# Kernel tuning notes

Measured on AMD Instinct MI355X. Metric: run time of the kernel, lower is better.

Reference implementation:

```python
import jax, jax.numpy as jnp
import numpy as np

B, T, D, M, N = 32, 24, 32, 32, 32
H = 32           # hidden_dim (must equal D due to .view in the torch code)
C = M * N        # number of independent per-cell LSTMs
K = 3            # conv kernel size, padding = K // 2


def setup_inputs() -> dict:
    key = jax.random.key(0)
    ks = jax.random.split(key, 7)
    s = 1.0 / np.sqrt(H)  # torch nn.LSTM default init scale
    return {
        "x": jax.random.normal(ks[0], (B, T, D, M, N), jnp.float32),
        "W_ih": jax.random.uniform(ks[1], (C, 4 * H, D), jnp.float32, -s, s),
        "W_hh": jax.random.uniform(ks[2], (C, 4 * H, H), jnp.float32, -s, s),
        "b_ih": jax.random.uniform(ks[3], (C, 4 * H), jnp.float32, -s, s),
        "b_hh": jax.random.uniform(ks[4], (C, 4 * H), jnp.float32, -s, s),
        "conv_w": jax.random.normal(ks[5], (1, H, K, K), jnp.float32) * 0.05,
        "conv_b": jax.random.normal(ks[6], (1,), jnp.float32) * 0.05,
    }


def _spatial_lstm(x, W_ih, W_hh, b_ih, b_hh):
    # x: (B,T,D,M,N) -> per-cell sequences (T,C,B,D)
    xf = x.reshape(B, T, D, C).transpose(1, 3, 0, 2)
    bias = (b_ih + b_hh)[:, None, :]  # (C,1,4H)

    def step(carry, xt):
        h, c = carry  # (C,B,H)
        g = (jnp.einsum('cbd,cgd->cbg', xt, W_ih)
             + jnp.einsum('cbh,cgh->cbg', h, W_hh) + bias)
        i, f, gg, o = jnp.split(g, 4, axis=-1)  # torch gate order i,f,g,o
        c = jax.nn.sigmoid(f) * c + jax.nn.sigmoid(i) * jnp.tanh(gg)
        h = jax.nn.sigmoid(o) * jnp.tanh(c)
        return (h, c), h

    h0 = jnp.zeros((C, B, H), x.dtype)
    _, hs = jax.lax.scan(step, (h0, h0), xf)  # hs: (T,C,B,H)
    # stack over cells, view back to grid: (B,T,H,M,N)
    return hs.transpose(2, 0, 3, 1).reshape(B, T, H, M, N)


def reference(x, W_ih, W_hh, b_ih, b_hh, conv_w, conv_b):
    spatial = _spatial_lstm(x, W_ih, W_hh, b_ih, b_hh)  # (B,T,H,M,N)
    y = jax.lax.conv_general_dilated(
        spatial.reshape(B * T, H, M, N), conv_w,
        window_strides=(1, 1), padding=[(K // 2, K // 2)] * 2,
        dimension_numbers=('NCHW', 'OIHW', 'NCHW'))
    y = y + conv_b[None, :, None, None]
    return jax.nn.sigmoid(y).reshape(B, T, -1, M, N)


if __name__ == "__main__":
    out = reference(**setup_inputs())
    print(out.shape)
```

## Files before the change

kernel.cpp:

```cpp
#include <hip/hip_runtime.h>

#define Bn 32
#define Tn 24
#define Dn 32
#define Hn 32
#define Cn 1024
#define DC (Dn*Cn)
#define TDC (Tn*Dn*Cn)
#define MP 34
#define PPXN (MP*MP)
#define IMGS (MP*MP*32)
#define SCALE 1.442695041f

typedef __attribute__((ext_vector_type(8))) short bf16x8;
typedef __attribute__((ext_vector_type(4))) float f32x4;

__device__ __forceinline__ unsigned cvt_pk(float lo, float hi) {
    unsigned r; asm("v_cvt_pk_bf16_f32 %0, %1, %2" : "=v"(r) : "v"(lo), "v"(hi)); return r;
}
__device__ __forceinline__ float lo16f(unsigned u) { return __builtin_bit_cast(float, u << 16); }
__device__ __forceinline__ float hi16f(unsigned u) { return __builtin_bit_cast(float, u & 0xffff0000u); }
__device__ __forceinline__ float rcp_(float x) { return __builtin_amdgcn_rcpf(x); }
__device__ __forceinline__ float exp2_(float x) { return __builtin_amdgcn_exp2f(x); }
__device__ __forceinline__ bf16x8 bc(int4 v) { return __builtin_bit_cast(bf16x8, v); }

struct __align__(16) LdsT {
    unsigned short Xh[2][2][32][48];
    unsigned short Xl[2][2][32][48];
    float Hf[2][2][32][36];
};

__global__ __launch_bounds__(512)
void zero_halo(unsigned short* __restrict__ sp) {
    int gid = blockIdx.x * 512 + threadIdx.x;
    if (gid >= 3072 * 132) return;
    int plane = gid / 132;
    int r = gid - plane * 132;
    int m, n;
    if (r < 34)       { m = 0;      n = r; }
    else if (r < 68)  { m = 33;     n = r - 34; }
    else if (r < 100) { m = r - 67; n = 0; }
    else              { m = r - 99; n = 33; }
    int4 z = {0, 0, 0, 0};
    *(int4*)(sp + ((size_t)plane * PPXN + m * MP + n) * 8) = z;
}

__global__ __launch_bounds__(256) __attribute__((amdgpu_waves_per_eu(3, 3)))
void lstm_k10(const float* __restrict__ x,
              const float* __restrict__ Wih,
              const float* __restrict__ Whh,
              const float* __restrict__ bih,
              const float* __restrict__ bhh,
              unsigned short* __restrict__ sp)
{
    __shared__ LdsT lds;
    const int tid  = threadIdx.x;
    const int lane = tid & 63;
    const int wave = tid >> 6;
    const int ci   = wave >> 1;
    const int half = wave & 1;
    const int l16  = lane & 15;
    const int kg   = lane >> 4;
    const int bid  = blockIdx.x;
    const int cellbase = (bid & 7) * 128 + (bid >> 3) * 2;
    const int cell = cellbase + ci;

    int4 wihh[4], wihl[4], whhh[4], whhl[4];
    float biasr[4];
#pragma unroll
    for (int q = 0; q < 4; ++q) {
        const int g = q * 32 + half * 16 + l16;
        const float* wp = Wih + (size_t)cell * 4096 + g * 32 + kg * 8;
        const float* hp = Whh + (size_t)cell * 4096 + g * 32 + kg * 8;
        float wv[8], hv[8];
#pragma unroll
        for (int j = 0; j < 8; ++j) { wv[j] = wp[j] * SCALE; hv[j] = hp[j] * SCALE; }
        unsigned a0 = cvt_pk(wv[0], wv[1]), a1 = cvt_pk(wv[2], wv[3]);
        unsigned a2 = cvt_pk(wv[4], wv[5]), a3 = cvt_pk(wv[6], wv[7]);
        wihh[q] = int4{(int)a0, (int)a1, (int)a2, (int)a3};
        wihl[q] = int4{(int)cvt_pk(wv[0] - lo16f(a0), wv[1] - hi16f(a0)),
                       (int)cvt_pk(wv[2] - lo16f(a1), wv[3] - hi16f(a1)),
                       (int)cvt_pk(wv[4] - lo16f(a2), wv[5] - hi16f(a2)),
                       (int)cvt_pk(wv[6] - lo16f(a3), wv[7] - hi16f(a3))};
        unsigned b0 = cvt_pk(hv[0], hv[1]), b1 = cvt_pk(hv[2], hv[3]);
        unsigned b2 = cvt_pk(hv[4], hv[5]), b3 = cvt_pk(hv[6], hv[7]);
        whhh[q] = int4{(int)b0, (int)b1, (int)b2, (int)b3};
        whhl[q] = int4{(int)cvt_pk(hv[0] - lo16f(b0), hv[1] - hi16f(b0)),
                       (int)cvt_pk(hv[2] - lo16f(b1), hv[3] - hi16f(b1)),
                       (int)cvt_pk(hv[4] - lo16f(b2), hv[5] - hi16f(b2)),
                       (int)cvt_pk(hv[6] - lo16f(b3), hv[7] - hi16f(b3))};
        biasr[q] = (bih[cell * 128 + g] + bhh[cell * 128 + g]) * SCALE;
    }

    const int sb = tid >> 3;
    const int d0 = (tid & 7) * 4;
    const float* xg0 = x + (size_t)sb * TDC + (size_t)d0 * Cn + cellbase;

    const int sm = cell >> 5, sn = cell & 31;
    const int ppx = (sm + 1) * MP + (sn + 1);
    unsigned short* spb = sp + ((size_t)(half * 16 + l16) * Tn * 4 + kg) * (PPXN * 8)
                             + (size_t)ppx * 8;

    float hD[8] = {};
    float cst[8] = {};
    float2 nx[4];
#pragma unroll
    for (int k = 0; k < 4; ++k) nx[k] = *(const float2*)(xg0 + k * Cn);

    for (int t = 0; t < Tn; ++t) {
        const int bufi = t & 1;
#pragma unroll
        for (int cc = 0; cc < 2; ++cc) {
            float f0 = cc ? nx[0].y : nx[0].x;
            float f1 = cc ? nx[1].y : nx[1].x;
            float f2 = cc ? nx[2].y : nx[2].x;
            float f3 = cc ? nx[3].y : nx[3].x;
            unsigned a0 = cvt_pk(f0, f1), a1 = cvt_pk(f2, f3);
            float r0 = f0 - lo16f(a0), r1 = f1 - hi16f(a0);
            float r2 = f2 - lo16f(a1), r3 = f3 - hi16f(a1);
            int2 hi2 = {(int)a0, (int)a1};
            int2 lo2 = {(int)cvt_pk(r0, r1), (int)cvt_pk(r2, r3)};
            *(int2*)&lds.Xh[bufi][cc][sb][d0] = hi2;
            *(int2*)&lds.Xl[bufi][cc][sb][d0] = lo2;
        }
#pragma unroll
        for (int i = 0; i < 8; ++i) {
            int mt = i >> 2, r = i & 3;
            lds.Hf[bufi][ci][mt * 16 + kg * 4 + r][half * 16 + l16] = hD[i];
        }
        if (t < Tn - 1) {
#pragma unroll
            for (int k = 0; k < 4; ++k)
                nx[k] = *(const float2*)(xg0 + (size_t)(t + 1) * DC + k * Cn);
        }
        __syncthreads();

        unsigned sphi0 = 0, sphi1 = 0, sphi2 = 0, sphi3 = 0;
#pragma unroll
        for (int mt = 0; mt < 2; ++mt) {
            int4 xfh = *(const int4*)&lds.Xh[bufi][ci][mt * 16 + l16][kg * 8];
            int4 xfl = *(const int4*)&lds.Xl[bufi][ci][mt * 16 + l16][kg * 8];
            const float* hp = &lds.Hf[bufi][ci][mt * 16 + l16][kg * 8];
            float4 ha = *(const float4*)hp;
            float4 hb = *(const float4*)(hp + 4);
            unsigned p0 = cvt_pk(ha.x, ha.y), p1 = cvt_pk(ha.z, ha.w);
            unsigned p2 = cvt_pk(hb.x, hb.y), p3 = cvt_pk(hb.z, hb.w);
            int4 hfh = int4{(int)p0, (int)p1, (int)p2, (int)p3};
            int4 hfl = int4{(int)cvt_pk(ha.x - lo16f(p0), ha.y - hi16f(p0)),
                            (int)cvt_pk(ha.z - lo16f(p1), ha.w - hi16f(p1)),
                            (int)cvt_pk(hb.x - lo16f(p2), hb.y - hi16f(p2)),
                            (int)cvt_pk(hb.z - lo16f(p3), hb.w - hi16f(p3))};
            if (mt == half) { sphi0 = p0; sphi1 = p1; sphi2 = p2; sphi3 = p3; }

            f32x4 acc[4];
#pragma unroll
            for (int q = 0; q < 4; ++q) {
                f32x4 a = {biasr[q], biasr[q], biasr[q], biasr[q]};
                a = __builtin_amdgcn_mfma_f32_16x16x32_bf16(bc(xfh), bc(wihh[q]), a, 0, 0, 0);
                a = __builtin_amdgcn_mfma_f32_16x16x32_bf16(bc(xfl), bc(wihh[q]), a, 0, 0, 0);
                a = __builtin_amdgcn_mfma_f32_16x16x32_bf16(bc(xfh), bc(wihl[q]), a, 0, 0, 0);
                a = __builtin_amdgcn_mfma_f32_16x16x32_bf16(bc(hfh), bc(whhh[q]), a, 0, 0, 0);
                a = __builtin_amdgcn_mfma_f32_16x16x32_bf16(bc(hfl), bc(whhh[q]), a, 0, 0, 0);
                a = __builtin_amdgcn_mfma_f32_16x16x32_bf16(bc(hfh), bc(whhl[q]), a, 0, 0, 0);
                acc[q] = a;
            }
#pragma unroll
            for (int r = 0; r < 4; ++r) {
                float gi = acc[0][r], gf = acc[1][r];
                float gg = acc[2][r], go = acc[3][r];
                float ig = rcp_(1.f + exp2_(-gi));
                float fg = rcp_(1.f + exp2_(-gf));
                float gt = 1.f - 2.f * rcp_(1.f + exp2_(gg + gg));
                float og = rcp_(1.f + exp2_(-go));
                float c  = fg * cst[mt * 4 + r] + ig * gt;
                cst[mt * 4 + r] = c;
                float tc = 1.f - 2.f * rcp_(1.f + exp2_((2.f * SCALE) * c));
                hD[mt * 4 + r] = og * tc;
            }
        }

        if (t > 0) {
            int4 sv = {(int)sphi0, (int)sphi1, (int)sphi2, (int)sphi3};
            *(int4*)(spb + (size_t)(t - 1) * IMGS) = sv;
        }
    }

#pragma unroll
    for (int i = 0; i < 8; ++i) {
        int mt = i >> 2, r = i & 3;
        lds.Hf[0][ci][mt * 16 + kg * 4 + r][half * 16 + l16] = hD[i];
    }
    __syncthreads();
    {
        const float* hp = &lds.Hf[0][ci][half * 16 + l16][kg * 8];
        float4 ha = *(const float4*)hp;
        float4 hb = *(const float4*)(hp + 4);
        int4 sv = {(int)cvt_pk(ha.x, ha.y), (int)cvt_pk(ha.z, ha.w),
                   (int)cvt_pk(hb.x, hb.y), (int)cvt_pk(hb.z, hb.w)};
        *(int4*)(spb + (size_t)(Tn - 1) * IMGS) = sv;
    }
}

__global__ __launch_bounds__(512, 4)
void conv_k4(const unsigned short* __restrict__ sp,
             const float* __restrict__ cw,
             const float* __restrict__ cb,
             float* __restrict__ out)
{
    __shared__ float wlds[9][32];
    const int tid = threadIdx.x;
    const int img = blockIdx.x;
    if (tid < 288) wlds[tid >> 5][tid & 31] = cw[(tid & 31) * 9 + (tid >> 5)];
    __syncthreads();
    const float bias = cb[0];
    float acc[2] = {bias, bias};
    int ppx[2];
#pragma unroll
    for (int pk = 0; pk < 2; ++pk) {
        int px = tid + pk * 512;
        ppx[pk] = ((px >> 5) + 1) * MP + (px & 31) + 1;
    }
#pragma unroll
    for (int hc = 0; hc < 4; ++hc) {
        float4 wa[9], wb[9];
#pragma unroll
        for (int tap = 0; tap < 9; ++tap) {
            wa[tap] = *(const float4*)&wlds[tap][hc * 8];
            wb[tap] = *(const float4*)&wlds[tap][hc * 8 + 4];
        }
        const unsigned short* plane = sp + (size_t)(img * 4 + hc) * (PPXN * 8);
#pragma unroll
        for (int pk = 0; pk < 2; ++pk) {
            const unsigned short* base = plane + (size_t)ppx[pk] * 8;
            float a = acc[pk];
#pragma unroll
            for (int dm = -1; dm <= 1; ++dm)
#pragma unroll
                for (int dn = -1; dn <= 1; ++dn) {
                    const int tap = (dm + 1) * 3 + (dn + 1);
                    int4 v = *(const int4*)(base + (dm * MP + dn) * 8);
                    float4 w0 = wa[tap], w1 = wb[tap];
                    a = fmaf(lo16f((unsigned)v.x), w0.x, a);
                    a = fmaf(hi16f((unsigned)v.x), w0.y, a);
                    a = fmaf(lo16f((unsigned)v.y), w0.z, a);
                    a = fmaf(hi16f((unsigned)v.y), w0.w, a);
                    a = fmaf(lo16f((unsigned)v.z), w1.x, a);
                    a = fmaf(hi16f((unsigned)v.z), w1.y, a);
                    a = fmaf(lo16f((unsigned)v.w), w1.z, a);
                    a = fmaf(hi16f((unsigned)v.w), w1.w, a);
                }
            acc[pk] = a;
        }
    }
#pragma unroll
    for (int pk = 0; pk < 2; ++pk)
        out[(size_t)img * 1024 + tid + pk * 512] = rcp_(1.f + exp2_(-SCALE * acc[pk]));
}

extern "C" void kernel_launch(void* const* d_in, const int* in_sizes, int n_in,
                              void* d_out, int out_size, void* d_ws, size_t ws_size,
                              hipStream_t stream) {
    const float* x   = (const float*)d_in[0];
    const float* Wih = (const float*)d_in[1];
    const float* Whh = (const float*)d_in[2];
    const float* bih = (const float*)d_in[3];
    const float* bhh = (const float*)d_in[4];
    const float* cw  = (const float*)d_in[5];
    const float* cb  = (const float*)d_in[6];
    float* out = (float*)d_out;
    unsigned short* sp = (unsigned short*)d_ws;

    zero_halo<<<792, 512, 0, stream>>>(sp);
    lstm_k10<<<512, 256, 0, stream>>>(x, Wih, Whh, bih, bhh, sp);
    conv_k4<<<Bn * Tn, 512, 0, stream>>>(sp, cw, cb, out);
}
```

Before: 101.6 us.

## Split LSTM batch across two blocks per cell pair to double grid parallelism

```diff
diff --git a/kernel.cpp b/kernel.cpp
--- a/kernel.cpp
+++ b/kernel.cpp
@@ -25,9 +25,9 @@
 __device__ __forceinline__ bf16x8 bc(int4 v) { return __builtin_bit_cast(bf16x8, v); }
 
 struct __align__(16) LdsT {
-    unsigned short Xh[2][2][32][48];
-    unsigned short Xl[2][2][32][48];
-    float Hf[2][2][32][36];
+    unsigned short Xh[2][2][16][48];
+    unsigned short Xl[2][2][16][48];
+    float Hf[2][2][16][36];
 };
 
 __global__ __launch_bounds__(512)
@@ -45,8 +45,8 @@
     *(int4*)(sp + ((size_t)plane * PPXN + m * MP + n) * 8) = z;
 }
 
-__global__ __launch_bounds__(256) __attribute__((amdgpu_waves_per_eu(3, 3)))
-void lstm_k10(const float* __restrict__ x,
+__global__ __launch_bounds__(256, 4)
+void lstm_k11(const float* __restrict__ x,
               const float* __restrict__ Wih,
               const float* __restrict__ Whh,
               const float* __restrict__ bih,
@@ -58,18 +58,22 @@
     const int lane = tid & 63;
     const int wave = tid >> 6;
     const int ci   = wave >> 1;
-    const int half = wave & 1;
+    const int gh   = wave & 1;
     const int l16  = lane & 15;
     const int kg   = lane >> 4;
     const int bid  = blockIdx.x;
-    const int cellbase = (bid & 7) * 128 + (bid >> 3) * 2;
+    const int xcd  = bid & 7, v = bid >> 3;
+    const int cg   = xcd * 64 + (v & 63);
+    const int bs   = v >> 6;
+    const int cellbase = cg * 2;
     const int cell = cellbase + ci;
+    const int gb0  = bs * 16;
 
     int4 wihh[4], wihl[4], whhh[4], whhl[4];
     float biasr[4];
 #pragma unroll
     for (int q = 0; q < 4; ++q) {
-        const int g = q * 32 + half * 16 + l16;
+        const int g = q * 32 + gh * 16 + l16;
         const float* wp = Wih + (size_t)cell * 4096 + g * 32 + kg * 8;
         const float* hp = Whh + (size_t)cell * 4096 + g * 32 + kg * 8;
         float wv[8], hv[8];
@@ -92,111 +96,95 @@
         biasr[q] = (bih[cell * 128 + g] + bhh[cell * 128 + g]) * SCALE;
     }
 
-    const int sb = tid >> 3;
-    const int d0 = (tid & 7) * 4;
-    const float* xg0 = x + (size_t)sb * TDC + (size_t)d0 * Cn + cellbase;
-
+    const int sb = tid >> 4;
+    const int d0 = (tid & 15) * 2;
+    const float* xg0 = x + (size_t)(gb0 + sb) * TDC + (size_t)d0 * Cn + cellbase;
+
+    const int b_loc = lane & 15, kg2 = lane >> 4;
     const int sm = cell >> 5, sn = cell & 31;
     const int ppx = (sm + 1) * MP + (sn + 1);
-    unsigned short* spb = sp + ((size_t)(half * 16 + l16) * Tn * 4 + kg) * (PPXN * 8)
-                             + (size_t)ppx * 8;
-
-    float hD[8] = {};
-    float cst[8] = {};
-    float2 nx[4];
-#pragma unroll
-    for (int k = 0; k < 4; ++k) nx[k] = *(const float2*)(xg0 + k * Cn);
+    unsigned short* spb = sp + (((size_t)(gb0 + b_loc) * (Tn * 4) + kg2) * PPXN + ppx) * 8;
+
+    float hD[4] = {}, cst[4] = {};
+    float2 nx0 = *(const float2*)xg0;
+    float2 nx1 = *(const float2*)(xg0 + Cn);
 
     for (int t = 0; t < Tn; ++t) {
         const int bufi = t & 1;
 #pragma unroll
         for (int cc = 0; cc < 2; ++cc) {
-            float f0 = cc ? nx[0].y : nx[0].x;
-            float f1 = cc ? nx[1].y : nx[1].x;
-            float f2 = cc ? nx[2].y : nx[2].x;
-            float f3 = cc ? nx[3].y : nx[3].x;
-            unsigned a0 = cvt_pk(f0, f1), a1 = cvt_pk(f2, f3);
-            float r0 = f0 - lo16f(a0), r1 = f1 - hi16f(a0);
-            float r2 = f2 - lo16f(a1), r3 = f3 - hi16f(a1);
-            int2 hi2 = {(int)a0, (int)a1};
-            int2 lo2 = {(int)cvt_pk(r0, r1), (int)cvt_pk(r2, r3)};
-            *(int2*)&lds.Xh[bufi][cc][sb][d0] = hi2;
-            *(int2*)&lds.Xl[bufi][cc][sb][d0] = lo2;
-        }
-#pragma unroll
-        for (int i = 0; i < 8; ++i) {
-            int mt = i >> 2, r = i & 3;
-            lds.Hf[bufi][ci][mt * 16 + kg * 4 + r][half * 16 + l16] = hD[i];
-        }
+            float f0 = cc ? nx0.y : nx0.x;
+            float f1 = cc ? nx1.y : nx1.x;
+            unsigned a0 = cvt_pk(f0, f1);
+            unsigned l0 = cvt_pk(f0 - lo16f(a0), f1 - hi16f(a0));
+            *(unsigned*)&lds.Xh[bufi][cc][sb][d0] = a0;
+            *(unsigned*)&lds.Xl[bufi][cc][sb][d0] = l0;
+        }
+#pragma unroll
+        for (int r = 0; r < 4; ++r)
+            lds.Hf[bufi][ci][kg * 4 + r][gh * 16 + l16] = hD[r];
         if (t < Tn - 1) {
-#pragma unroll
-            for (int k = 0; k < 4; ++k)
-                nx[k] = *(const float2*)(xg0 + (size_t)(t + 1) * DC + k * Cn);
+            nx0 = *(const float2*)(xg0 + (size_t)(t + 1) * DC);
+            nx1 = *(const float2*)(xg0 + (size_t)(t + 1) * DC + Cn);
         }
         __syncthreads();
 
-        unsigned sphi0 = 0, sphi1 = 0, sphi2 = 0, sphi3 = 0;
-#pragma unroll
-        for (int mt = 0; mt < 2; ++mt) {
-            int4 xfh = *(const int4*)&lds.Xh[bufi][ci][mt * 16 + l16][kg * 8];
-            int4 xfl = *(const int4*)&lds.Xl[bufi][ci][mt * 16 + l16][kg * 8];
-            const float* hp = &lds.Hf[bufi][ci][mt * 16 + l16][kg * 8];
-            float4 ha = *(const float4*)hp;
-            float4 hb = *(const float4*)(hp + 4);
-            unsigned p0 = cvt_pk(ha.x, ha.y), p1 = cvt_pk(ha.z, ha.w);
-            unsigned p2 = cvt_pk(hb.x, hb.y), p3 = cvt_pk(hb.z, hb.w);
-            int4 hfh = int4{(int)p0, (int)p1, (int)p2, (int)p3};
-            int4 hfl = int4{(int)cvt_pk(ha.x - lo16f(p0), ha.y - hi16f(p0)),
-                            (int)cvt_pk(ha.z - lo16f(p1), ha.w - hi16f(p1)),
-                            (int)cvt_pk(hb.x - lo16f(p2), hb.y - hi16f(p2)),
-                            (int)cvt_pk(hb.z - lo16f(p3), hb.w - hi16f(p3))};
-            if (mt == half) { sphi0 = p0; sphi1 = p1; sphi2 = p2; sphi3 = p3; }
-
-            f32x4 acc[4];
-#pragma unroll
-            for (int q = 0; q < 4; ++q) {
-                f32x4 a = {biasr[q], biasr[q], biasr[q], biasr[q]};
-                a = __builtin_amdgcn_mfma_f32_16x16x32_bf16(bc(xfh), bc(wihh[q]), a, 0, 0, 0);
-                a = __builtin_amdgcn_mfma_f32_16x16x32_bf16(bc(xfl), bc(wihh[q]), a, 0, 0, 0);
-                a = __builtin_amdgcn_mfma_f32_16x16x32_bf16(bc(xfh), bc(wihl[q]), a, 0, 0, 0);
-                a = __builtin_amdgcn_mfma_f32_16x16x32_bf16(bc(hfh), bc(whhh[q]), a, 0, 0, 0);
-                a = __builtin_amdgcn_mfma_f32_16x16x32_bf16(bc(hfl), bc(whhh[q]), a, 0, 0, 0);
-                a = __builtin_amdgcn_mfma_f32_16x16x32_bf16(bc(hfh), bc(whhl[q]), a, 0, 0, 0);
-                acc[q] = a;
-            }
-#pragma unroll
-            for (int r = 0; r < 4; ++r) {
-                float gi = acc[0][r], gf = acc[1][r];
-                float gg = acc[2][r], go = acc[3][r];
-                float ig = rcp_(1.f + exp2_(-gi));
-                float fg = rcp_(1.f + exp2_(-gf));
-                float gt = 1.f - 2.f * rcp_(1.f + exp2_(gg + gg));
-                float og = rcp_(1.f + exp2_(-go));
-                float c  = fg * cst[mt * 4 + r] + ig * gt;
-                cst[mt * 4 + r] = c;
-                float tc = 1.f - 2.f * rcp_(1.f + exp2_((2.f * SCALE) * c));
-                hD[mt * 4 + r] = og * tc;
-            }
-        }
-
-        if (t > 0) {
-            int4 sv = {(int)sphi0, (int)sphi1, (int)sphi2, (int)sphi3};
-            *(int4*)(spb + (size_t)(t - 1) * IMGS) = sv;
-        }
-    }
-
-#pragma unroll
-    for (int i = 0; i < 8; ++i) {
-        int mt = i >> 2, r = i & 3;
-        lds.Hf[0][ci][mt * 16 + kg * 4 + r][half * 16 + l16] = hD[i];
-    }
-    __syncthreads();
-    {
-        const float* hp = &lds.Hf[0][ci][half * 16 + l16][kg * 8];
+        int4 xfh = *(const int4*)&lds.Xh[bufi][ci][l16][kg * 8];
+        int4 xfl = *(const int4*)&lds.Xl[bufi][ci][l16][kg * 8];
+        const float* hp = &lds.Hf[bufi][ci][l16][kg * 8];
         float4 ha = *(const float4*)hp;
         float4 hb = *(const float4*)(hp + 4);
-        int4 sv = {(int)cvt_pk(ha.x, ha.y), (int)cvt_pk(ha.z, ha.w),
-                   (int)cvt_pk(hb.x, hb.y), (int)cvt_pk(hb.z, hb.w)};
+        unsigned p0 = cvt_pk(ha.x, ha.y), p1 = cvt_pk(ha.z, ha.w);
+        unsigned p2 = cvt_pk(hb.x, hb.y), p3 = cvt_pk(hb.z, hb.w);
+        int4 hfh = int4{(int)p0, (int)p1, (int)p2, (int)p3};
+        int4 hfl = int4{(int)cvt_pk(ha.x - lo16f(p0), ha.y - hi16f(p0)),
+                        (int)cvt_pk(ha.z - lo16f(p1), ha.w - hi16f(p1)),
+                        (int)cvt_pk(hb.x - lo16f(p2), hb.y - hi16f(p2)),
+                        (int)cvt_pk(hb.z - lo16f(p3), hb.w - hi16f(p3))};
+
+        if (gh == 0 && t > 0) {
+            int4 sv = {(int)p0, (int)p1, (int)p2, (int)p3};
+            *(int4*)(spb + (size_t)(t - 1) * IMGS) = sv;
+        }
+
+        f32x4 acc[4];
+#pragma unroll
+        for (int q = 0; q < 4; ++q) {
+            f32x4 a = {biasr[q], biasr[q], biasr[q], biasr[q]};
+            a = __builtin_amdgcn_mfma_f32_16x16x32_bf16(bc(xfh), bc(wihh[q]), a, 0, 0, 0);
+            a = __builtin_amdgcn_mfma_f32_16x16x32_bf16(bc(xfl), bc(wihh[q]), a, 0, 0, 0);
+            a = __builtin_amdgcn_mfma_f32_16x16x32_bf16(bc(xfh), bc(wihl[q]), a, 0, 0, 0);
+            a = __builtin_amdgcn_mfma_f32_16x16x32_bf16(bc(hfh), bc(whhh[q]), a, 0, 0, 0);
+            a = __builtin_amdgcn_mfma_f32_16x16x32_bf16(bc(hfl), bc(whhh[q]), a, 0, 0, 0);
+            a = __builtin_amdgcn_mfma_f32_16x16x32_bf16(bc(hfh), bc(whhl[q]), a, 0, 0, 0);
+            acc[q] = a;
+        }
+
+#pragma unroll
+        for (int r = 0; r < 4; ++r) {
+            float gi = acc[0][r], gf = acc[1][r];
+            float gg = acc[2][r], go = acc[3][r];
+            float ig = rcp_(1.f + exp2_(-gi));
+            float fg = rcp_(1.f + exp2_(-gf));
+            float gt = 1.f - 2.f * rcp_(1.f + exp2_(gg + gg));
+            float og = rcp_(1.f + exp2_(-go));
+            float c  = fg * cst[r] + ig * gt;
+            cst[r] = c;
+            float tc = 1.f - 2.f * rcp_(1.f + exp2_((2.f * SCALE) * c));
+            hD[r] = og * tc;
+        }
+    }
+
+#pragma unroll
+    for (int r = 0; r < 4; ++r)
+        lds.Hf[0][ci][kg * 4 + r][gh * 16 + l16] = hD[r];
+    __syncthreads();
+    if (gh == 0) {
+        const float* hq = &lds.Hf[0][ci][l16][kg * 8];
+        float4 ea = *(const float4*)hq;
+        float4 eb = *(const float4*)(hq + 4);
+        int4 sv = {(int)cvt_pk(ea.x, ea.y), (int)cvt_pk(ea.z, ea.w),
+                   (int)cvt_pk(eb.x, eb.y), (int)cvt_pk(eb.z, eb.w)};
         *(int4*)(spb + (size_t)(Tn - 1) * IMGS) = sv;
     }
 }
@@ -271,6 +259,6 @@
     unsigned short* sp = (unsigned short*)d_ws;
 
     zero_halo<<<792, 512, 0, stream>>>(sp);
-    lstm_k10<<<512, 256, 0, stream>>>(x, Wih, Whh, bih, bhh, sp);
+    lstm_k11<<<1024, 256, 0, stream>>>(x, Wih, Whh, bih, bhh, sp);
     conv_k4<<<Bn * Tn, 512, 0, stream>>>(sp, cw, cb, out);
 }
```

Result: slower. 113.4 us (+11.7%).
